# Performance work log

Measured on AMD Instinct MI355X. Metric: run time of the kernel, lower is better.

The kernel has to match this reference:

```python
import jax, jax.numpy as jnp
import numpy as np

N, E, H, C, G = 10000, 20000, 12, 768, 64  # nodes, edges, heads, per-head dim, graphs
NEG_SLOPE = 0.2


def _gat_layer(x, W, a_src, a_dst, b, src, dst):
    # x: [N, 768], W: [768, H*C], a_src/a_dst: [H, C], b: [C]
    h = (x @ W).reshape(-1, H, C)                      # [N, H, C]
    s = jnp.einsum('nhc,hc->nh', h, a_src)             # alpha_src per node
    d = jnp.einsum('nhc,hc->nh', h, a_dst)             # alpha_dst per node
    e = jax.nn.leaky_relu(s[src] + d[dst], NEG_SLOPE)  # [Etot, H]
    # segment softmax over incoming edges of each destination node
    m = jax.lax.stop_gradient(jax.ops.segment_max(e, dst, num_segments=N))
    ex = jnp.exp(e - m[dst])
    den = jax.ops.segment_sum(ex, dst, num_segments=N)
    alpha = ex / (den[dst] + 1e-16)                    # [Etot, H]
    out = jax.ops.segment_sum(h[src] * alpha[:, :, None], dst, num_segments=N)
    return out.mean(axis=1) + b                        # concat=False -> head mean, [N, C]


def setup_inputs() -> dict:
    key = jax.random.key(0)
    ks = jax.random.split(key, 16)
    sc = 0.02
    f32 = jnp.float32
    return {
        'x': jax.random.normal(ks[0], (N, 768), f32),
        'edge_index': jax.random.randint(ks[1], (2, E), 0, N),
        'batch': jnp.sort(jax.random.randint(ks[2], (N,), 0, G)),
        'W1': (jax.random.normal(ks[3], (768, H * C), f32) * sc),
        'a_src1': (jax.random.normal(ks[4], (H, C), f32) * sc),
        'a_dst1': (jax.random.normal(ks[5], (H, C), f32) * sc),
        'b1': jnp.zeros((C,), f32),
        'W2': (jax.random.normal(ks[6], (768, H * C), f32) * sc),
        'a_src2': (jax.random.normal(ks[7], (H, C), f32) * sc),
        'a_dst2': (jax.random.normal(ks[8], (H, C), f32) * sc),
        'b2': jnp.zeros((C,), f32),
        'mlp_w1': (jax.random.normal(ks[9], (768, 128), f32) * sc),
        'mlp_b1': jnp.zeros((128,), f32),
        'mlp_w2': (jax.random.normal(ks[10], (128, 4), f32) * sc),
        'mlp_b2': jnp.zeros((4,), f32),
    }


def reference(x, edge_index, batch, W1, a_src1, a_dst1, b1, W2, a_src2, a_dst2, b2,
              mlp_w1, mlp_b1, mlp_w2, mlp_b2):
    loops = jnp.arange(N)                               # GATConv add_self_loops=True
    src = jnp.concatenate([edge_index[0], loops])
    dst = jnp.concatenate([edge_index[1], loops])
    h = _gat_layer(x, W1, a_src1, a_dst1, b1, src, dst)
    h = _gat_layer(h, W2, a_src2, a_dst2, b2, src, dst)
    # scatter_mean over graph assignment
    ssum = jax.ops.segment_sum(h, batch, num_segments=G)
    cnt = jax.ops.segment_sum(jnp.ones((N,), h.dtype), batch, num_segments=G)
    g = ssum / jnp.maximum(cnt, 1.0)[:, None]           # [G, 768]
    z = jax.nn.relu(g @ mlp_w1 + mlp_b1)
    return z @ mlp_w2 + mlp_b2                          # [G, 4] logits
```

## Files before the change

### kernel.cpp

```cpp
#include <hip/hip_runtime.h>
#include <stdint.h>

typedef unsigned short u16;
typedef unsigned int   u32;

#define NNODES 10000
#define NEDGES 20000
#define ETOT   30000
#define NHEADS 12
#define CDIM   768
#define FDIM   768
#define KDIM   9216
#define NGRAPH 64
#define MPAD   10112
#define KT     24
#define NEG_SLOPE 0.2f
#define DMAX   32

typedef __attribute__((ext_vector_type(8))) short short8;
typedef __attribute__((ext_vector_type(4))) float f32x4;

__device__ __forceinline__ u16 f32_bf16(float f) {
  u32 u = __float_as_uint(f);
  u = (u + 0x7FFFu + ((u >> 16) & 1u)) >> 16;
  return (u16)u;
}
__device__ __forceinline__ float bf16_f32(u16 v) {
  return __uint_as_float(((u32)v) << 16);
}


__global__ void k_count(const int* __restrict__ dste, int* __restrict__ counts) {
  int e = blockIdx.x * blockDim.x + threadIdx.x;
  if (e >= ETOT) return;
  int dst;
  if (e < NEDGES) dst = dste[e]; else dst = e - NEDGES;
  atomicAdd(&counts[dst], 1);
}

__global__ void k_scan(const int* __restrict__ counts, int* __restrict__ offs) {
  __shared__ int part[256];
  int t = threadIdx.x;
  const int chunk = 40;
  int beg = t * chunk;
  int end = beg + chunk; if (end > NNODES) end = NNODES;
  int s = 0;
  for (int i = beg; i < end && i < NNODES; i++) s += counts[i];
  part[t] = s;
  __syncthreads();
  for (int d = 1; d < 256; d <<= 1) {
    int v = (t >= d) ? part[t - d] : 0;
    __syncthreads();
    part[t] += v;
    __syncthreads();
  }
  int base = (t == 0) ? 0 : part[t - 1];
  for (int i = beg; i < end && i < NNODES; i++) { offs[i] = base; base += counts[i]; }
  if (t == 255) offs[NNODES] = base;
}

__global__ void k_seed(const int* __restrict__ offs, int* __restrict__ cursor) {
  int n = blockIdx.x * blockDim.x + threadIdx.x;
  if (n < NNODES) cursor[n] = offs[n];
}

__global__ void k_scatter(const int* __restrict__ dste, int* __restrict__ cursor,
                          int* __restrict__ elist) {
  int e = blockIdx.x * blockDim.x + threadIdx.x;
  if (e >= ETOT) return;
  int dst;
  if (e < NEDGES) dst = dste[e]; else dst = e - NEDGES;
  int pos = atomicAdd(&cursor[dst], 1);
  elist[pos] = e;
}

__global__ void k_U(const float* __restrict__ W, const float* __restrict__ a_src,
                    const float* __restrict__ a_dst, float* __restrict__ Ut) {
  int k = blockIdx.x;
  int t = threadIdx.x, w = t >> 6, l = t & 63;
  const float* Wrow = W + (size_t)k * KDIM;
#pragma unroll
  for (int q = 0; q < 6; q++) {
    int o = w * 6 + q;
    int h = (o < 12) ? o : o - 12;
    const float* av = (o < 12) ? (a_src + h * CDIM) : (a_dst + h * CDIM);
    const float* wr = Wrow + h * CDIM;
    float p = 0.f;
    for (int c = l; c < CDIM; c += 64) p += wr[c] * av[c];
#pragma unroll
    for (int d = 32; d > 0; d >>= 1) p += __shfl_down(p, d, 64);
    if (l == 0) Ut[o * FDIM + k] = p;
  }
}

__global__ void k_sd(const float* __restrict__ xin, const float* __restrict__ Ut,
                     float* __restrict__ sd, u16* __restrict__ Ap) {
  __shared__ float UtS[24 * FDIM];
  int t = threadIdx.x, w = t >> 6, l = t & 63;
  const float4* U4 = (const float4*)Ut;
  float4* S4 = (float4*)UtS;
  for (int i = t; i < 24 * FDIM / 4; i += 256) S4[i] = U4[i];
  __syncthreads();
#pragma unroll
  for (int rep = 0; rep < 5; rep++) {
    int n = blockIdx.x * 20 + w * 5 + rep;
    if (n >= NNODES) continue;
    const float* xr = xin + (size_t)n * FDIM;
    float4 x0 = *(const float4*)(xr + 4 * l);
    float4 x1 = *(const float4*)(xr + 4 * l + 256);
    float4 x2 = *(const float4*)(xr + 4 * l + 512);
    int fr = n >> 4, rl = n & 15;
    float4 xv[3] = {x0, x1, x2};
#pragma unroll
    for (int c = 0; c < 3; c++) {
      int k0 = 4 * l + c * 256;
      ushort4 pk;
      pk.x = f32_bf16(xv[c].x); pk.y = f32_bf16(xv[c].y);
      pk.z = f32_bf16(xv[c].z); pk.w = f32_bf16(xv[c].w);
      u16* dst = Ap + ((size_t)fr * KT + (k0 >> 5)) * 512
               + ((rl + 16 * ((k0 >> 3) & 3)) << 3) + (k0 & 7);
      *(ushort4*)dst = pk;
    }
#pragma unroll
    for (int o = 0; o < 24; o++) {
      const float4* up = (const float4*)(UtS + o * FDIM + 4 * l);
      float4 u0 = up[0];
      float4 u1 = up[64];
      float4 u2 = up[128];
      float a = x0.x * u0.x + x0.y * u0.y + x0.z * u0.z + x0.w * u0.w
              + x1.x * u1.x + x1.y * u1.y + x1.z * u1.z + x1.w * u1.w
              + x2.x * u2.x + x2.y * u2.y + x2.z * u2.z + x2.w * u2.w;
#pragma unroll
      for (int d = 32; d > 0; d >>= 1) a += __shfl_xor(a, d, 64);
      if (l == 0) sd[n * 24 + o] = a;
    }
  }
}

__global__ void k_trans(const float* __restrict__ W, u16* __restrict__ Bp) {
  int kt = blockIdx.x * 32, jt = blockIdx.y * 32;
  int tx = threadIdx.x, ty = threadIdx.y;
  __shared__ float tile[32][33];
#pragma unroll
  for (int r = 0; r < 4; r++)
    tile[ty + 8 * r][tx] = W[(size_t)(kt + ty + 8 * r) * KDIM + jt + tx];
  __syncthreads();
  int j = jt + tx;
  int k0 = kt + 4 * ty;
  ushort4 pk;
  pk.x = f32_bf16(tile[4 * ty + 0][tx]);
  pk.y = f32_bf16(tile[4 * ty + 1][tx]);
  pk.z = f32_bf16(tile[4 * ty + 2][tx]);
  pk.w = f32_bf16(tile[4 * ty + 3][tx]);
  u16* dst = Bp + ((size_t)(j >> 4) * KT + (k0 >> 5)) * 512
           + (((j & 15) + 16 * ((k0 >> 3) & 3)) << 3) + (k0 & 7);
  *(ushort4*)dst = pk;
}

__global__ __launch_bounds__(256, 2) void k_gemm(const u16* __restrict__ Ap,
    const u16* __restrict__ Bp, u16* __restrict__ C) {
  int t = threadIdx.x;
  int w = t >> 6, l = t & 63;
  int col0 = blockIdx.x * 256;
  int row0 = blockIdx.y * 128;
  int wm = (w >> 1) * 64;
  int wn = (w & 1) * 128;
  const short8* Av = (const short8*)Ap + l;
  const short8* Bv = (const short8*)Bp + l;
  int fA = ((row0 + wm) >> 4) * KT;
  int fB = ((col0 + wn) >> 4) * KT;
  f32x4 acc[4][8] = {};

  for (int kt = 0; kt < KT; kt++) {
    short8 a0 = Av[(size_t)(fA + 0 * KT + kt) * 64];
    short8 a1 = Av[(size_t)(fA + 1 * KT + kt) * 64];
    short8 a2 = Av[(size_t)(fA + 2 * KT + kt) * 64];
    short8 a3 = Av[(size_t)(fA + 3 * KT + kt) * 64];
    short8 b0 = Bv[(size_t)(fB + 0 * KT + kt) * 64];
    short8 b1 = Bv[(size_t)(fB + 1 * KT + kt) * 64];
    short8 b2 = Bv[(size_t)(fB + 2 * KT + kt) * 64];
    short8 b3 = Bv[(size_t)(fB + 3 * KT + kt) * 64];
    short8 b4 = Bv[(size_t)(fB + 4 * KT + kt) * 64];
    short8 b5 = Bv[(size_t)(fB + 5 * KT + kt) * 64];
    short8 b6 = Bv[(size_t)(fB + 6 * KT + kt) * 64];
    short8 b7 = Bv[(size_t)(fB + 7 * KT + kt) * 64];
    short8 av[4] = {a0, a1, a2, a3};
    short8 bv[8] = {b0, b1, b2, b3, b4, b5, b6, b7};
#pragma unroll
    for (int i = 0; i < 4; i++)
#pragma unroll
      for (int j = 0; j < 8; j++)
        acc[i][j] = __builtin_amdgcn_mfma_f32_16x16x32_bf16(av[i], bv[j], acc[i][j], 0, 0, 0);
  }

  int lr = l & 15, lg = l >> 4;
#pragma unroll
  for (int i = 0; i < 4; i++)
#pragma unroll
    for (int j = 0; j < 8; j++) {
      int col = col0 + wn + j * 16 + lr;
#pragma unroll
      for (int r = 0; r < 4; r++) {
        int row = row0 + wm + i * 16 + lg * 4 + r;
        C[(size_t)row * KDIM + col] = f32_bf16(acc[i][j][r]);
      }
    }
}

__global__ void k_att(const u16* __restrict__ Hbig, const int* __restrict__ ei,
                      const int* __restrict__ offs, const int* __restrict__ elist,
                      const float* __restrict__ sd, const float* __restrict__ bias,
                      float* __restrict__ out) {
  int t = threadIdx.x, w = t >> 6, l = t & 63;
  int n = blockIdx.x * 4 + w;
  __shared__ int   srcsS[4][DMAX];
  __shared__ float alphS[4][NHEADS * DMAX];
  if (n >= NNODES) return;
  int* srcs = srcsS[w];
  float* alph = alphS[w];
  int beg = offs[n];
  int deg = offs[n + 1] - beg;
  if (deg > DMAX) deg = DMAX;
  if (l < deg) {
    int e = elist[beg + l];
    srcs[l] = (e < NEDGES) ? ei[e] : e - NEDGES;
  }
  __builtin_amdgcn_wave_barrier();
  for (int p = l; p < deg * NHEADS; p += 64) {
    int i = p / NHEADS, h = p - i * NHEADS;
    float v = sd[srcs[i] * 24 + h] + sd[n * 24 + 12 + h];
    v = (v > 0.f) ? v : NEG_SLOPE * v;
    alph[h * DMAX + i] = v;
  }
  __builtin_amdgcn_wave_barrier();
  if (l < NHEADS) {
    float m = -1e30f;
    for (int i = 0; i < deg; i++) m = fmaxf(m, alph[l * DMAX + i]);
    float s = 0.f;
    for (int i = 0; i < deg; i++) {
      float ex = expf(alph[l * DMAX + i] - m);
      alph[l * DMAX + i] = ex;
      s += ex;
    }
    float inv = 1.f / (s + 1e-16f);
    for (int i = 0; i < deg; i++) alph[l * DMAX + i] *= inv;
  }
  __builtin_amdgcn_wave_barrier();
#pragma unroll
  for (int pass = 0; pass < 3; pass++) {
    float4 acc = make_float4(0.f, 0.f, 0.f, 0.f);
    for (int i = 0; i < deg; i++) {
      const u16* hb = Hbig + (size_t)srcs[i] * KDIM + pass * 256 + 4 * l;
#pragma unroll
      for (int h = 0; h < NHEADS; h++) {
        ushort4 hv = *(const ushort4*)(hb + h * CDIM);
        float a = alph[h * DMAX + i];
        acc.x += a * bf16_f32(hv.x);
        acc.y += a * bf16_f32(hv.y);
        acc.z += a * bf16_f32(hv.z);
        acc.w += a * bf16_f32(hv.w);
      }
    }
    int c = pass * 256 + 4 * l;
    const float sc = 1.f / 12.f;
    float4 ov;
    ov.x = acc.x * sc + bias[c + 0];
    ov.y = acc.y * sc + bias[c + 1];
    ov.z = acc.z * sc + bias[c + 2];
    ov.w = acc.w * sc + bias[c + 3];
    *(float4*)(out + (size_t)n * FDIM + c) = ov;
  }
}

__global__ void k_pool(const float* __restrict__ h2, const int* __restrict__ batch,
                       float* __restrict__ g) {
  int gi = blockIdx.x;
  int c = blockIdx.y * 256 + threadIdx.x;
  int lo = 0, hi = NNODES;
  while (lo < hi) { int mid = (lo + hi) >> 1; if (batch[mid] < gi) lo = mid + 1; else hi = mid; }
  int start = lo;
  lo = start; hi = NNODES;
  while (lo < hi) { int mid = (lo + hi) >> 1; if (batch[mid] < gi + 1) lo = mid + 1; else hi = mid; }
  int end = lo;
  int cnt = end - start; if (cnt < 1) cnt = 1;
  float inv = 1.f / (float)cnt;
  float s = 0.f;
  for (int n = start; n < end; n++) s += h2[(size_t)n * FDIM + c];
  g[gi * FDIM + c] = s * inv;
}

__global__ void k_mlp(const float* __restrict__ g, const float* __restrict__ w1,
                      const float* __restrict__ b1, const float* __restrict__ w2,
                      const float* __restrict__ b2, float* __restrict__ out) {
  int gi = blockIdx.x;
  int t = threadIdx.x;
  __shared__ float gs[FDIM];
  __shared__ float zs[128];
  for (int i = t; i < FDIM; i += 128) gs[i] = g[gi * FDIM + i];
  __syncthreads();
  float a = b1[t];
  for (int k = 0; k < FDIM; k++) a += gs[k] * w1[k * 128 + t];
  zs[t] = (a > 0.f) ? a : 0.f;
  __syncthreads();
  if (t < 4) {
    float o = b2[t];
    for (int i = 0; i < 128; i++) o += zs[i] * w2[i * 4 + t];
    out[gi * 4 + t] = o;
  }
}

extern "C" void kernel_launch(void* const* d_in, const int* in_sizes, int n_in,
                              void* d_out, int out_size, void* d_ws, size_t ws_size,
                              hipStream_t stream) {
  const float* x    = (const float*)d_in[0];
  const int*   ei   = (const int*)d_in[1];
  const int*   batch= (const int*)d_in[2];
  const float* W1   = (const float*)d_in[3];
  const float* as1  = (const float*)d_in[4];
  const float* ad1  = (const float*)d_in[5];
  const float* b1   = (const float*)d_in[6];
  const float* W2   = (const float*)d_in[7];
  const float* as2  = (const float*)d_in[8];
  const float* ad2  = (const float*)d_in[9];
  const float* b2   = (const float*)d_in[10];
  const float* mw1  = (const float*)d_in[11];
  const float* mb1  = (const float*)d_in[12];
  const float* mw2  = (const float*)d_in[13];
  const float* mb2  = (const float*)d_in[14];
  float* out = (float*)d_out;
  (void)in_sizes; (void)n_in; (void)out_size; (void)ws_size;

  char* wsb = (char*)d_ws;
  size_t off = 0;
  auto alloc = [&](size_t bytes) -> void* {
    void* p = wsb + off;
    off += (bytes + 255) & ~(size_t)255;
    return p;
  };
  u16*  Hbig   = (u16*)alloc((size_t)MPAD * KDIM * 2);
  u16*  Bp     = (u16*)alloc((size_t)KDIM * FDIM * 2);
  float* h1    = (float*)alloc((size_t)NNODES * FDIM * 4);
  float* h2    = (float*)alloc((size_t)NNODES * FDIM * 4);
  u16*  Ap     = (u16*)h2;
  float* sd    = (float*)alloc((size_t)NNODES * 24 * 4);
  float* Ut    = (float*)alloc((size_t)FDIM * 24 * 4);
  int*  counts = (int*)alloc((size_t)NNODES * 4);
  int*  offs   = (int*)alloc((size_t)(NNODES + 1) * 4);
  int*  cursor = (int*)alloc((size_t)NNODES * 4);
  int*  elist  = (int*)alloc((size_t)ETOT * 4);
  float* gbuf  = (float*)alloc((size_t)NGRAPH * FDIM * 4);

  hipMemsetAsync(counts, 0, NNODES * 4, stream);
  k_count<<<(ETOT + 255) / 256, 256, 0, stream>>>(ei + NEDGES, counts);
  k_scan<<<1, 256, 0, stream>>>(counts, offs);
  k_seed<<<(NNODES + 255) / 256, 256, 0, stream>>>(offs, cursor);
  k_scatter<<<(ETOT + 255) / 256, 256, 0, stream>>>(ei + NEDGES, cursor, elist);

  for (int layer = 0; layer < 2; layer++) {
    const float* xin  = layer ? h1  : x;
    const float* W    = layer ? W2  : W1;
    const float* asrc = layer ? as2 : as1;
    const float* adst = layer ? ad2 : ad1;
    const float* bb   = layer ? b2  : b1;
    float* hout       = layer ? h2  : h1;

    k_U<<<FDIM, 256, 0, stream>>>(W, asrc, adst, Ut);
    k_sd<<<(NNODES + 19) / 20, 256, 0, stream>>>(xin, Ut, sd, Ap);
    k_trans<<<dim3(FDIM / 32, KDIM / 32), dim3(32, 8), 0, stream>>>(W, Bp);
    k_gemm<<<dim3(KDIM / 256, MPAD / 128), 256, 0, stream>>>(Ap, Bp, Hbig);
    k_att<<<(NNODES + 3) / 4, 256, 0, stream>>>(Hbig, ei, offs, elist, sd, bb, hout);
  }

  k_pool<<<dim3(NGRAPH, 3), 256, 0, stream>>>(h2, batch, gbuf);
  k_mlp<<<NGRAPH, 128, 0, stream>>>(gbuf, mw1, mb1, mw2, mb2, out);
}
```

Measured before the change: 888.3 us.

## Split attention into softmax and source-major scatter with atomic accumulation

Attention aggregation moves from a destination-gather to a source-major scatter. A new kernel computes the softmax coefficients per edge into a buffer. A second kernel loads each source node's 12-head row once and atomically adds the weighted sums into every destination, after the outputs are initialised with the bias. A second CSR keyed by source is built for this. The aim is to read each Hbig row once instead of once per incoming edge, at the cost of float atomics, extra launches and non-deterministic summation order.

```diff
diff --git a/kernel.cpp b/kernel.cpp
--- a/kernel.cpp
+++ b/kernel.cpp
@@ -30,12 +30,12 @@
 }
 
 
-__global__ void k_count(const int* __restrict__ dste, int* __restrict__ counts) {
+__global__ void k_count(const int* __restrict__ keye, int* __restrict__ counts) {
   int e = blockIdx.x * blockDim.x + threadIdx.x;
   if (e >= ETOT) return;
-  int dst;
-  if (e < NEDGES) dst = dste[e]; else dst = e - NEDGES;
-  atomicAdd(&counts[dst], 1);
+  int key;
+  if (e < NEDGES) key = keye[e]; else key = e - NEDGES;
+  atomicAdd(&counts[key], 1);
 }
 
 __global__ void k_scan(const int* __restrict__ counts, int* __restrict__ offs) {
@@ -64,13 +64,13 @@
   if (n < NNODES) cursor[n] = offs[n];
 }
 
-__global__ void k_scatter(const int* __restrict__ dste, int* __restrict__ cursor,
+__global__ void k_scatter(const int* __restrict__ keye, int* __restrict__ cursor,
                           int* __restrict__ elist) {
   int e = blockIdx.x * blockDim.x + threadIdx.x;
   if (e >= ETOT) return;
-  int dst;
-  if (e < NEDGES) dst = dste[e]; else dst = e - NEDGES;
-  int pos = atomicAdd(&cursor[dst], 1);
+  int key;
+  if (e < NEDGES) key = keye[e]; else key = e - NEDGES;
+  int pos = atomicAdd(&cursor[key], 1);
   elist[pos] = e;
 }
 
@@ -207,28 +207,26 @@
     }
 }
 
-__global__ void k_att(const u16* __restrict__ Hbig, const int* __restrict__ ei,
-                      const int* __restrict__ offs, const int* __restrict__ elist,
-                      const float* __restrict__ sd, const float* __restrict__ bias,
-                      float* __restrict__ out) {
+__global__ void k_soft(const int* __restrict__ ei, const int* __restrict__ offs,
+                       const int* __restrict__ elist, const float* __restrict__ sd,
+                       float* __restrict__ ebuf) {
   int t = threadIdx.x, w = t >> 6, l = t & 63;
   int n = blockIdx.x * 4 + w;
-  __shared__ int   srcsS[4][DMAX];
+  __shared__ int   eidS[4][DMAX];
   __shared__ float alphS[4][NHEADS * DMAX];
   if (n >= NNODES) return;
-  int* srcs = srcsS[w];
+  int* eid = eidS[w];
   float* alph = alphS[w];
   int beg = offs[n];
   int deg = offs[n + 1] - beg;
   if (deg > DMAX) deg = DMAX;
-  if (l < deg) {
-    int e = elist[beg + l];
-    srcs[l] = (e < NEDGES) ? ei[e] : e - NEDGES;
-  }
+  if (l < deg) eid[l] = elist[beg + l];
   __builtin_amdgcn_wave_barrier();
   for (int p = l; p < deg * NHEADS; p += 64) {
     int i = p / NHEADS, h = p - i * NHEADS;
-    float v = sd[srcs[i] * 24 + h] + sd[n * 24 + 12 + h];
+    int e = eid[i];
+    int src = (e < NEDGES) ? ei[e] : e - NEDGES;
+    float v = sd[src * 24 + h] + sd[n * 24 + 12 + h];
     v = (v > 0.f) ? v : NEG_SLOPE * v;
     alph[h * DMAX + i] = v;
   }
@@ -246,29 +244,50 @@
     for (int i = 0; i < deg; i++) alph[l * DMAX + i] *= inv;
   }
   __builtin_amdgcn_wave_barrier();
+  for (int p = l; p < deg * NHEADS; p += 64) {
+    int i = p / NHEADS, h = p - i * NHEADS;
+    ebuf[(size_t)eid[i] * NHEADS + h] = alph[h * DMAX + i];
+  }
+}
+
+__global__ void k_binit(const float* __restrict__ bias, float* __restrict__ out) {
+  int n = blockIdx.x, t = threadIdx.x;
+  *(float4*)(out + (size_t)n * FDIM + 4 * t) = *(const float4*)(bias + 4 * t);
+}
+
+__global__ void k_scat(const u16* __restrict__ Hbig, const int* __restrict__ ei,
+                       const int* __restrict__ soffs, const int* __restrict__ selist,
+                       const float* __restrict__ ebuf, float* __restrict__ out) {
+  int t = threadIdx.x, w = t >> 6, l = t & 63;
+  int n = blockIdx.x * 4 + w;
+  if (n >= NNODES) return;
+  int beg = soffs[n], end = soffs[n + 1];
+  const float sc = 1.f / 12.f;
 #pragma unroll
   for (int pass = 0; pass < 3; pass++) {
-    float4 acc = make_float4(0.f, 0.f, 0.f, 0.f);
-    for (int i = 0; i < deg; i++) {
-      const u16* hb = Hbig + (size_t)srcs[i] * KDIM + pass * 256 + 4 * l;
+    const u16* hb = Hbig + (size_t)n * KDIM + pass * 256 + 4 * l;
+    ushort4 hv[NHEADS];
+#pragma unroll
+    for (int h = 0; h < NHEADS; h++) hv[h] = *(const ushort4*)(hb + h * CDIM);
+    for (int idx = beg; idx < end; idx++) {
+      int e = selist[idx];
+      int dst = (e < NEDGES) ? ei[NEDGES + e] : e - NEDGES;
+      const float* ar = ebuf + (size_t)e * NHEADS;
+      float4 acc = make_float4(0.f, 0.f, 0.f, 0.f);
 #pragma unroll
       for (int h = 0; h < NHEADS; h++) {
-        ushort4 hv = *(const ushort4*)(hb + h * CDIM);
-        float a = alph[h * DMAX + i];
-        acc.x += a * bf16_f32(hv.x);
-        acc.y += a * bf16_f32(hv.y);
-        acc.z += a * bf16_f32(hv.z);
-        acc.w += a * bf16_f32(hv.w);
+        float a = ar[h];
+        acc.x += a * bf16_f32(hv[h].x);
+        acc.y += a * bf16_f32(hv[h].y);
+        acc.z += a * bf16_f32(hv[h].z);
+        acc.w += a * bf16_f32(hv[h].w);
       }
+      float* op = out + (size_t)dst * FDIM + pass * 256 + 4 * l;
+      unsafeAtomicAdd(op + 0, acc.x * sc);
+      unsafeAtomicAdd(op + 1, acc.y * sc);
+      unsafeAtomicAdd(op + 2, acc.z * sc);
+      unsafeAtomicAdd(op + 3, acc.w * sc);
     }
-    int c = pass * 256 + 4 * l;
-    const float sc = 1.f / 12.f;
-    float4 ov;
-    ov.x = acc.x * sc + bias[c + 0];
-    ov.y = acc.y * sc + bias[c + 1];
-    ov.z = acc.z * sc + bias[c + 2];
-    ov.w = acc.w * sc + bias[c + 3];
-    *(float4*)(out + (size_t)n * FDIM + c) = ov;
   }
 }
 
@@ -344,17 +363,24 @@
   u16*  Ap     = (u16*)h2;
   float* sd    = (float*)alloc((size_t)NNODES * 24 * 4);
   float* Ut    = (float*)alloc((size_t)FDIM * 24 * 4);
+  float* ebuf  = (float*)alloc((size_t)ETOT * NHEADS * 4);
   int*  counts = (int*)alloc((size_t)NNODES * 4);
   int*  offs   = (int*)alloc((size_t)(NNODES + 1) * 4);
-  int*  cursor = (int*)alloc((size_t)NNODES * 4);
   int*  elist  = (int*)alloc((size_t)ETOT * 4);
+  int*  soffs  = (int*)alloc((size_t)(NNODES + 1) * 4);
+  int*  selist = (int*)alloc((size_t)ETOT * 4);
   float* gbuf  = (float*)alloc((size_t)NGRAPH * FDIM * 4);
 
   hipMemsetAsync(counts, 0, NNODES * 4, stream);
   k_count<<<(ETOT + 255) / 256, 256, 0, stream>>>(ei + NEDGES, counts);
   k_scan<<<1, 256, 0, stream>>>(counts, offs);
-  k_seed<<<(NNODES + 255) / 256, 256, 0, stream>>>(offs, cursor);
-  k_scatter<<<(ETOT + 255) / 256, 256, 0, stream>>>(ei + NEDGES, cursor, elist);
+  k_seed<<<(NNODES + 255) / 256, 256, 0, stream>>>(offs, counts);
+  k_scatter<<<(ETOT + 255) / 256, 256, 0, stream>>>(ei + NEDGES, counts, elist);
+  hipMemsetAsync(counts, 0, NNODES * 4, stream);
+  k_count<<<(ETOT + 255) / 256, 256, 0, stream>>>(ei, counts);
+  k_scan<<<1, 256, 0, stream>>>(counts, soffs);
+  k_seed<<<(NNODES + 255) / 256, 256, 0, stream>>>(soffs, counts);
+  k_scatter<<<(ETOT + 255) / 256, 256, 0, stream>>>(ei, counts, selist);
 
   for (int layer = 0; layer < 2; layer++) {
     const float* xin  = layer ? h1  : x;
@@ -368,7 +394,9 @@
     k_sd<<<(NNODES + 19) / 20, 256, 0, stream>>>(xin, Ut, sd, Ap);
     k_trans<<<dim3(FDIM / 32, KDIM / 32), dim3(32, 8), 0, stream>>>(W, Bp);
     k_gemm<<<dim3(KDIM / 256, MPAD / 128), 256, 0, stream>>>(Ap, Bp, Hbig);
-    k_att<<<(NNODES + 3) / 4, 256, 0, stream>>>(Hbig, ei, offs, elist, sd, bb, hout);
+    k_soft<<<(NNODES + 3) / 4, 256, 0, stream>>>(ei, offs, elist, sd, ebuf);
+    k_binit<<<NNODES, 192, 0, stream>>>(bb, hout);
+    k_scat<<<(NNODES + 3) / 4, 256, 0, stream>>>(Hbig, ei, soffs, selist, ebuf, hout);
   }
 
   k_pool<<<dim3(NGRAPH, 3), 256, 0, stream>>>(h2, batch, gbuf);
```

Result: slower. 1.403 ms (+58.0%).
